# Optimization experiments

Measured on AMD Instinct MI355X. Metric: run time of the kernel, lower is better.

Reference implementation:

```python
import jax, jax.numpy as jnp
import numpy as np

LN_EPS = 1e-5


def _layer_norm(h, g, b):
    mu = jnp.mean(h, axis=-1, keepdims=True)
    var = jnp.mean((h - mu) ** 2, axis=-1, keepdims=True)
    return (h - mu) / jnp.sqrt(var + LN_EPS) * g + b


def setup_inputs() -> dict:
    key = jax.random.key(0)
    ks = jax.random.split(key, 12)
    B, N, D = 2, 2048, 768
    H, Dh = 12, 64
    Dp = D // 4  # 192, DynamicPositionBias width
    s = lambda fan_in: 1.0 / np.sqrt(fan_in)
    return {
        "x": jax.random.normal(ks[0], (B, N, D), jnp.float32),
        "qkv_w": jax.random.normal(ks[1], (D, 3 * H * Dh), jnp.float32) * s(D),
        "qkv_b": jax.random.normal(ks[2], (3 * H * Dh,), jnp.float32) * 0.02,
        "out_w": jax.random.normal(ks[3], (H * Dh, D), jnp.float32) * s(H * Dh),
        "out_b": jax.random.normal(ks[4], (D,), jnp.float32) * 0.02,
        "dpb_w_in": jax.random.normal(ks[5], (1, Dp), jnp.float32),
        "dpb_b_in": jax.random.normal(ks[6], (Dp,), jnp.float32) * 0.02,
        "dpb_w_hid": jax.random.normal(ks[7], (3, Dp, Dp), jnp.float32) * s(Dp),
        "dpb_b_hid": jax.random.normal(ks[8], (3, Dp), jnp.float32) * 0.02,
        "dpb_ln_g": jnp.ones((4, Dp), jnp.float32),
        "dpb_ln_b": jnp.zeros((4, Dp), jnp.float32),
        "dpb_w_out": jax.random.normal(ks[9], (Dp, 12), jnp.float32) * s(Dp),
        "dpb_b_out": jax.random.normal(ks[10], (12,), jnp.float32) * 0.02,
    }


def _dpb_bias(n, w_in, b_in, w_hid, b_hid, ln_g, ln_b, w_out, b_out):
    # positions -n+1 .. n-1, log-distance transform
    pos = jnp.arange(-n + 1, n, dtype=jnp.float32)[:, None]  # [2n-1, 1]
    pos = jnp.sign(pos) * jnp.log(jnp.abs(pos) + 1.0)
    h = jax.nn.silu(_layer_norm(pos @ w_in + b_in, ln_g[0], ln_b[0]))
    for l in range(3):
        h = jax.nn.silu(_layer_norm(h @ w_hid[l] + b_hid[l], ln_g[l + 1], ln_b[l + 1]))
    vals = h @ w_out + b_out  # [2n-1, H]
    idx = jnp.arange(n)[:, None] - jnp.arange(n)[None, :] + (n - 1)  # [n, n]
    bias = vals[idx]  # [n, n, H]
    return jnp.transpose(bias, (2, 0, 1))  # [H, n, n]


def reference(x, qkv_w, qkv_b, out_w, out_b,
              dpb_w_in, dpb_b_in, dpb_w_hid, dpb_b_hid,
              dpb_ln_g, dpb_ln_b, dpb_w_out, dpb_b_out):
    B, N, D = x.shape
    H = dpb_w_out.shape[-1]
    qkv = x @ qkv_w + qkv_b  # [B, N, 3*H*Dh]
    q, k, v = jnp.split(qkv, 3, axis=-1)
    split_heads = lambda t: jnp.transpose(t.reshape(B, N, H, -1), (0, 2, 1, 3))
    q, k, v = split_heads(q), split_heads(k), split_heads(v)  # [B, H, N, Dh]
    Dh = q.shape[-1]

    bias = _dpb_bias(N, dpb_w_in, dpb_b_in, dpb_w_hid, dpb_b_hid,
                     dpb_ln_g, dpb_ln_b, dpb_w_out, dpb_b_out)  # [H, N, N]

    scale = Dh ** -0.5
    sim = jnp.einsum("bhid,bhjd->bhij", q, k) * scale + bias[None]
    attn = jax.nn.softmax(sim, axis=-1)
    o = jnp.einsum("bhij,bhjd->bhid", attn, v)  # [B, H, N, Dh]
    o = jnp.transpose(o, (0, 2, 1, 3)).reshape(B, N, H * Dh)
    return o @ out_w + out_b
```

## Files before the change

### kernel.cpp

```cpp
#include <hip/hip_runtime.h>
#include <stdint.h>
#include <stddef.h>

typedef __bf16 bf16;
typedef __bf16 bf16x8 __attribute__((ext_vector_type(8)));
typedef float floatx4 __attribute__((ext_vector_type(4)));

typedef __attribute__((address_space(1))) void as1_void;
typedef __attribute__((address_space(3))) void as3_void;

__device__ __forceinline__ void async_ld16(const void* g, void* l) {
    __builtin_amdgcn_global_load_lds((as1_void*)g, (as3_void*)l, 16, 0, 0);
}

__device__ __forceinline__ floatx4 mfma16(bf16x8 a, bf16x8 b, floatx4 c) {
    return __builtin_amdgcn_mfma_f32_16x16x32_bf16(a, b, c, 0, 0, 0);
}

__device__ __forceinline__ unsigned cvtpk_bf16(float lo, float hi) {
    unsigned r;
    asm("v_cvt_pk_bf16_f32 %0, %1, %2" : "=v"(r) : "v"(lo), "v"(hi));
    return r;
}
__device__ __forceinline__ void pl32swap(unsigned &a, unsigned &b) {
    asm("v_permlane32_swap_b32 %0, %1" : "+v"(a), "+v"(b));
}
__device__ __forceinline__ void pl16swap(unsigned &a, unsigned &b) {
    asm("v_permlane16_swap_b32 %0, %1" : "+v"(a), "+v"(b));
}

#define LOG2E 1.4426950408889634f
#define SM_M2 24.0f
#define DP 192

__device__ __forceinline__ float ldsc(const void* p, size_t i, int isbf) {
    return isbf ? (float)((const bf16*)p)[i] : ((const float*)p)[i];
}
__device__ __forceinline__ bf16x8 ld8(const void* p, size_t i, int isbf) {
    if (isbf) return *(const bf16x8*)((const bf16*)p + i);
    const float* f = (const float*)p + i;
    float4 lo = *(const float4*)(f);
    float4 hi = *(const float4*)(f + 4);
    bf16x8 r;
    r[0]=(bf16)lo.x; r[1]=(bf16)lo.y; r[2]=(bf16)lo.z; r[3]=(bf16)lo.w;
    r[4]=(bf16)hi.x; r[5]=(bf16)hi.y; r[6]=(bf16)hi.z; r[7]=(bf16)hi.w;
    return r;
}
__device__ __forceinline__ int get_fl(const uint32_t* lng) {
    return (lng[0] == 0x3F803F80u) ? 1 : 0;
}

__device__ void transpose_body(const void* in, bf16* out, int R, int C,
                               int bx, int by, int fl, bf16 (*tile)[65]) {
    int c0 = bx * 64, r0 = by * 64;
    for (int i = threadIdx.x; i < 512; i += 256) {
        int rr = i >> 3, cc8 = (i & 7) * 8;
        int gr = r0 + rr, gc = c0 + cc8;
        if (gr < R && gc + 7 < C) {
            bf16x8 v = ld8(in, (size_t)gr * C + gc, fl);
            #pragma unroll
            for (int e = 0; e < 8; e++) tile[rr][cc8 + e] = v[e];
        } else {
            #pragma unroll
            for (int e = 0; e < 8; e++) {
                int gce = gc + e;
                tile[rr][cc8 + e] = (gr < R && gce < C)
                    ? (bf16)ldsc(in, (size_t)gr * C + gce, fl) : (bf16)0.0f;
            }
        }
    }
    __syncthreads();
    for (int i = threadIdx.x; i < 512; i += 256) {
        int cc = i >> 3, rr8 = (i & 7) * 8;
        int oR = c0 + cc, oC = r0 + rr8;
        if (oR < C && oC + 7 < R) {
            bf16x8 v;
            #pragma unroll
            for (int e = 0; e < 8; e++) v[e] = tile[rr8 + e][cc];
            *(bf16x8*)(out + (size_t)oR * R + oC) = v;
        } else if (oR < C) {
            #pragma unroll
            for (int e = 0; e < 8; e++)
                if (oC + e < R) out[(size_t)oR * R + oC + e] = tile[rr8 + e][cc];
        }
    }
}

__global__ __launch_bounds__(256) void prep_kernel(
    const void* __restrict__ qkv_w, const void* __restrict__ out_w,
    bf16* __restrict__ wt_qkv, bf16* __restrict__ wt_out,
    const void* __restrict__ w_hid, const void* __restrict__ w_out,
    bf16* __restrict__ WtH, bf16* __restrict__ Wt12,
    const uint32_t* __restrict__ lngw,
    const void* __restrict__ x, bf16* __restrict__ xbf)
{
    __shared__ bf16 tile[64][65];
    const int fl = get_fl(lngw);
    const int bid = blockIdx.x;
    if (bid < 432) {
        transpose_body(qkv_w, wt_qkv, 768, 2304, bid % 36, bid / 36, fl, tile);
        return;
    }
    if (bid < 576) {
        int b2 = bid - 432;
        transpose_body(out_w, wt_out, 768, 768, b2 % 12, b2 / 12, fl, tile);
        return;
    }
    if (bid < 603) {
        int b2 = bid - 576, l = b2 / 9, t9 = b2 % 9;
        transpose_body((const char*)w_hid + (size_t)l * DP * DP * (fl ? 2 : 4),
                       WtH + (size_t)l * DP * DP, DP, DP, t9 % 3, t9 / 3,
                       fl, tile);
        return;
    }
    if (bid < 606) {
        transpose_body(w_out, Wt12, 192, 12, 0, bid - 603, fl, tile);
        return;
    }
    size_t base = (size_t)(bid - 606) * 6144 + threadIdx.x * 8;
    #pragma unroll
    for (int c = 0; c < 3; c++)
        *(bf16x8*)(xbf + base + c*2048) = ld8(x, base + c*2048, fl);
}

#define GK 768
#define HS 200

__global__ __launch_bounds__(256) void gemm0_dpb_kernel(
    const bf16* __restrict__ A, const bf16* __restrict__ Bt,
    const void* __restrict__ bias, const uint32_t* __restrict__ lngw,
    bf16* __restrict__ out0, bf16* __restrict__ out1, bf16* __restrict__ out2,
    const void* __restrict__ w_in, const void* __restrict__ b_in,
    const void* __restrict__ b_hid, const void* __restrict__ ln_g,
    const void* __restrict__ ln_b, const void* __restrict__ b_out,
    const bf16* __restrict__ WtH, const bf16* __restrict__ Wt12,
    float* __restrict__ vals_t)
{
    __shared__ __align__(16) char smem[32768];
    const int fl = get_fl(lngw);
    const int tid = threadIdx.x;
    const int wave = tid >> 6, lane = tid & 63;
    const int g = lane >> 4, cl = lane & 15;

    if (blockIdx.x >= 576) {
        bf16*  Hb   = (bf16*)smem;
        float* redS = (float*)(smem + 6400);
        float* redQ = (float*)(smem + 6656);
        const int pbase = (blockIdx.x - 576) * 16;

        float tpos[4];
        #pragma unroll
        for (int rg = 0; rg < 4; rg++) {
            int p = pbase + g*4 + rg;
            float pv = (float)p - 2047.0f;
            float sg = (pv > 0.0f) ? 1.0f : ((pv < 0.0f) ? -1.0f : 0.0f);
            tpos[rg] = sg * logf(fabsf(pv) + 1.0f);
        }
        int col[3];
        #pragma unroll
        for (int tt = 0; tt < 3; tt++) col[tt] = (wave*3 + tt)*16 + cl;

        floatx4 acc[3];
        #pragma unroll
        for (int tt = 0; tt < 3; tt++) {
            float wi = ldsc(w_in, col[tt], fl), bi = ldsc(b_in, col[tt], fl);
            #pragma unroll
            for (int rg = 0; rg < 4; rg++) acc[tt][rg] = tpos[rg]*wi + bi;
        }

        #pragma unroll 1
        for (int l = 0; l < 4; l++) {
            float s1[4], s2[4];
            #pragma unroll
            for (int rg = 0; rg < 4; rg++) {
                s1[rg] = acc[0][rg] + acc[1][rg] + acc[2][rg];
                s2[rg] = acc[0][rg]*acc[0][rg] + acc[1][rg]*acc[1][rg]
                       + acc[2][rg]*acc[2][rg];
            }
            #pragma unroll
            for (int m = 1; m <= 8; m <<= 1)
                #pragma unroll
                for (int rg = 0; rg < 4; rg++) {
                    s1[rg] += __shfl_xor(s1[rg], m);
                    s2[rg] += __shfl_xor(s2[rg], m);
                }
            if (cl == 0)
                #pragma unroll
                for (int rg = 0; rg < 4; rg++) {
                    redS[wave*16 + g*4 + rg] = s1[rg];
                    redQ[wave*16 + g*4 + rg] = s2[rg];
                }
            __syncthreads();
            float mu[4], rstd[4];
            #pragma unroll
            for (int rg = 0; rg < 4; rg++) {
                int row = g*4 + rg;
                float S = redS[row] + redS[16+row] + redS[32+row] + redS[48+row];
                float Q = redQ[row] + redQ[16+row] + redQ[32+row] + redQ[48+row];
                float m_ = S * (1.0f/DP);
                float v_ = Q * (1.0f/DP) - m_*m_;
                mu[rg] = m_;
                rstd[rg] = 1.0f / sqrtf(v_ + 1e-5f);
            }
            #pragma unroll
            for (int tt = 0; tt < 3; tt++) {
                float ga = ldsc(ln_g, l*DP + col[tt], fl);
                float be = ldsc(ln_b, l*DP + col[tt], fl);
                #pragma unroll
                for (int rg = 0; rg < 4; rg++) {
                    float y = (acc[tt][rg] - mu[rg]) * rstd[rg] * ga + be;
                    float sil = y / (1.0f + __expf(-y));
                    Hb[(g*4 + rg)*HS + col[tt]] = (bf16)sil;
                }
            }
            __syncthreads();
            if (l == 3) break;
            #pragma unroll
            for (int tt = 0; tt < 3; tt++) {
                float bh = ldsc(b_hid, l*DP + col[tt], fl);
                #pragma unroll
                for (int rg = 0; rg < 4; rg++) acc[tt][rg] = bh;
            }
            const bf16* Wl = WtH + (size_t)l * DP * DP;
            #pragma unroll
            for (int ks = 0; ks < 6; ks++) {
                bf16x8 af = *(const bf16x8*)(Hb + cl*HS + ks*32 + g*8);
                #pragma unroll
                for (int tt = 0; tt < 3; tt++) {
                    bf16x8 bfv = *(const bf16x8*)(Wl + (size_t)col[tt]*DP
                                                  + ks*32 + g*8);
                    acc[tt] = mfma16(af, bfv, acc[tt]);
                }
            }
        }
        if (wave == 0) {
            floatx4 facc = {};
            if (cl < 12) {
                float bo = ldsc(b_out, cl, fl);
                #pragma unroll
                for (int rg = 0; rg < 4; rg++) facc[rg] = bo;
            }
            #pragma unroll
            for (int ks = 0; ks < 6; ks++) {
                bf16x8 af = *(const bf16x8*)(Hb + cl*HS + ks*32 + g*8);
                bf16x8 bfv = {};
                if (cl < 12)
                    bfv = *(const bf16x8*)(Wt12 + (size_t)cl*DP + ks*32 + g*8);
                facc = mfma16(af, bfv, facc);
            }
            if (cl < 12)
                #pragma unroll
                for (int rg = 0; rg < 4; rg++) {
                    int p = pbase + g*4 + rg;
                    if (p < 4095) vals_t[cl*4095 + p] = facc[rg];
                }
        }
        return;
    }

    bf16* Sb = (bf16*)smem;
    const int xcd8 = blockIdx.x & 7, slot = blockIdx.x >> 3;
    const int m0 = (xcd8*4 + slot/18) * 128, n0 = (slot % 18) * 128;
    const int wm = (wave >> 1) * 64, wn = (wave & 1) * 64;

    const int e0 = wave*512 + lane*8;
    const int e1 = e0 + 2048;
    const int r0 = e0 >> 5, c0e = e0 & 31;
    const int r1 = e1 >> 5, c1e = e1 & 31;
    const bf16* Ag0 = A  + (size_t)(m0 + r0) * GK + c0e;
    const bf16* Ag1 = A  + (size_t)(m0 + r1) * GK + c1e;
    const bf16* Bg0 = Bt + (size_t)(n0 + r0) * GK + c0e;
    const bf16* Bg1 = Bt + (size_t)(n0 + r1) * GK + c1e;

    const int frow = lane & 15, fk = (lane >> 4) * 8;
    floatx4 acc[4][4] = {};

    auto stage = [&](int t, int p) {
        const int k0 = t * 32;
        bf16* d = Sb + p * 8192;
        async_ld16(Ag0 + k0, d + e0);
        async_ld16(Ag1 + k0, d + e1);
        async_ld16(Bg0 + k0, d + 4096 + e0);
        async_ld16(Bg1 + k0, d + 4096 + e1);
    };

    stage(0, 0);
    __syncthreads();
    for (int t = 0; t < GK/32; ++t) {
        const int cur = t & 1;
        if (t + 1 < GK/32) stage(t + 1, cur ^ 1);
        const bf16* Ac = Sb + cur*8192;
        const bf16* Bc = Ac + 4096;
        bf16x8 af[4], bfr[4];
        #pragma unroll
        for (int i = 0; i < 4; i++)
            af[i] = *(const bf16x8*)(Ac + (wm + i*16 + frow)*32 + fk);
        #pragma unroll
        for (int j = 0; j < 4; j++)
            bfr[j] = *(const bf16x8*)(Bc + (wn + j*16 + frow)*32 + fk);
        #pragma unroll
        for (int i = 0; i < 4; i++)
            #pragma unroll
            for (int j = 0; j < 4; j++)
                acc[i][j] = mfma16(af[i], bfr[j], acc[i][j]);
        __syncthreads();
    }

    if (n0 >= 1536) {
        #pragma unroll
        for (int j = 0; j < 4; j++) {
            int Cc = n0 + wn + j*16 + cl;
            float bv = ldsc(bias, Cc, fl);
            int c2 = Cc - 1536, hh = c2 >> 6, dd = c2 & 63;
            #pragma unroll
            for (int kst = 0; kst < 2; kst++) {
                unsigned e0p = cvtpk_bf16(acc[2*kst][j][0] + bv,
                                          acc[2*kst][j][1] + bv);
                unsigned e1p = cvtpk_bf16(acc[2*kst][j][2] + bv,
                                          acc[2*kst][j][3] + bv);
                unsigned f0p = cvtpk_bf16(acc[2*kst+1][j][0] + bv,
                                          acc[2*kst+1][j][1] + bv);
                unsigned f1p = cvtpk_bf16(acc[2*kst+1][j][2] + bv,
                                          acc[2*kst+1][j][3] + bv);
                pl32swap(e0p, f0p); pl16swap(e0p, f0p);
                pl32swap(e1p, f1p); pl16swap(e1p, f1p);
                union { unsigned u[4]; bf16x8 v; } uu;
                uu.u[0] = e0p; uu.u[1] = e1p; uu.u[2] = f0p; uu.u[3] = f1p;
                int R0 = m0 + wm + kst*32 + g*8;
                int bb = R0 >> 11, nn = R0 & 2047;
                *(bf16x8*)(out2 + (((size_t)(bb*12 + hh) * 64 + dd) * 2048)
                           + nn) = uu.v;
            }
        }
        return;
    }

    #pragma unroll
    for (int i = 0; i < 4; i++) {
        #pragma unroll
        for (int j = 0; j < 4; j++) {
            int Cc = n0 + wn + j*16 + cl;
            float bv = ldsc(bias, Cc, fl);
            #pragma unroll
            for (int rg = 0; rg < 4; rg++) {
                int R = m0 + wm + i*16 + g*4 + rg;
                float val = acc[i][j][rg] + bv;
                int which = Cc / 768;
                int c2 = Cc - which * 768;
                int hh = c2 >> 6, dd = c2 & 63;
                int bb = R >> 11, nn = R & 2047;
                bf16* dst = (which == 0) ? out0 : out1;
                dst[((size_t)(bb*12 + hh) * 2048 + nn) * 64 + dd] = (bf16)val;
            }
        }
    }
}

__global__ __launch_bounds__(256) void gemm_out(
    const bf16* __restrict__ A, const bf16* __restrict__ Bt,
    const void* __restrict__ bias, const uint32_t* __restrict__ lngw,
    void* __restrict__ out0)
{
    __shared__ __align__(16) bf16 Sb[2][4096];
    const int fl  = get_fl(lngw);
    const int tid = threadIdx.x;
    const int wave = tid >> 6, lane = tid & 63;
    const int m0 = blockIdx.y * 64, n0 = blockIdx.x * 64;
    const int wm = (wave >> 1) * 32, wn = (wave & 1) * 32;

    const int e0 = tid * 8;
    const int r0 = e0 >> 5, c0e = e0 & 31;
    const bf16* Ag0 = A  + (size_t)(m0 + r0) * GK + c0e;
    const bf16* Bg0 = Bt + (size_t)(n0 + r0) * GK + c0e;

    const int frow = lane & 15, fk = (lane >> 4) * 8;
    floatx4 acc[2][2] = {};

    auto stage = [&](int t, int p) {
        const int k0 = t * 32;
        async_ld16(Ag0 + k0, &Sb[p][e0]);
        async_ld16(Bg0 + k0, &Sb[p][2048 + e0]);
    };

    stage(0, 0);
    __syncthreads();
    for (int t = 0; t < GK/32; ++t) {
        const int cur = t & 1;
        if (t + 1 < GK/32) stage(t + 1, cur ^ 1);
        const bf16* Ac = Sb[cur];
        const bf16* Bc = Ac + 2048;
        bf16x8 af[2], bfr[2];
        #pragma unroll
        for (int i = 0; i < 2; i++)
            af[i] = *(const bf16x8*)(Ac + (wm + i*16 + frow)*32 + fk);
        #pragma unroll
        for (int j = 0; j < 2; j++)
            bfr[j] = *(const bf16x8*)(Bc + (wn + j*16 + frow)*32 + fk);
        #pragma unroll
        for (int i = 0; i < 2; i++)
            #pragma unroll
            for (int j = 0; j < 2; j++)
                acc[i][j] = mfma16(af[i], bfr[j], acc[i][j]);
        __syncthreads();
    }

    const int g = lane >> 4, cl = lane & 15;
    #pragma unroll
    for (int i = 0; i < 2; i++) {
        #pragma unroll
        for (int j = 0; j < 2; j++) {
            int Cc = n0 + wn + j*16 + cl;
            float bv = ldsc(bias, Cc, fl);
            #pragma unroll
            for (int rg = 0; rg < 4; rg++) {
                int R = m0 + wm + i*16 + g*4 + rg;
                float val = acc[i][j][rg] + bv;
                size_t oi = (size_t)R * 768 + Cc;
                if (fl) ((bf16*)out0)[oi]  = (bf16)val;
                else    ((float*)out0)[oi] = val;
            }
        }
    }
}

__global__ __launch_bounds__(256) void attn_kernel(
    const bf16* __restrict__ qws, const bf16* __restrict__ kws,
    const bf16* __restrict__ vwst, const float* __restrict__ vals_t,
    bf16* __restrict__ ows)
{
    __shared__ __align__(16) bf16 Qs[64*72];
    __shared__ __align__(16) bf16 Ks[2][64*72];
    __shared__ __align__(16) bf16 Vt[2][64*72];
    __shared__ float bias_s[2][128];

    const int tid = threadIdx.x;
    const int wave = tid >> 6, lane = tid & 63;
    const int g = lane >> 4, cl = lane & 15;
    const int xcd8 = blockIdx.x & 7, slot = blockIdx.x >> 3;
    const int bh_ = xcd8*3 + (slot >> 5);
    const int q0 = (slot & 31) * 64;
    const int h = bh_ % 12, b = bh_ / 12;
    const size_t bh = (size_t)bh_;
    const bf16* qp  = qws  + bh * 2048 * 64;
    const bf16* kp  = kws  + bh * 2048 * 64;
    const bf16* vpt = vwst + bh * 64 * 2048;
    const float* vrow = vals_t + h * 4095;

    for (int i = tid; i < 512; i += 256) {
        int r = i >> 3, c = (i & 7) * 8;
        *(bf16x8*)(Qs + r*72 + c) = *(const bf16x8*)(qp + (size_t)(q0 + r)*64 + c);
    }

    const int sr0 = tid >> 3, sc0 = (tid & 7) * 8;
    const int sr1 = sr0 + 32;

    bf16x8 kreg0 = *(const bf16x8*)(kp + (size_t)sr0 * 64 + sc0);
    bf16x8 kreg1 = *(const bf16x8*)(kp + (size_t)sr1 * 64 + sc0);
    bf16x8 vreg0 = *(const bf16x8*)(vpt + (size_t)sr0 * 2048 + sc0);
    bf16x8 vreg1 = *(const bf16x8*)(vpt + (size_t)sr1 * 2048 + sc0);
    float  breg  = 0.0f;
    if (tid < 127) breg = vrow[q0 + 1984 + tid];
    *(bf16x8*)(Ks[0] + sr0*72 + sc0) = kreg0;
    *(bf16x8*)(Ks[0] + sr1*72 + sc0) = kreg1;
    *(bf16x8*)(Vt[0] + sr0*72 + sc0) = vreg0;
    *(bf16x8*)(Vt[0] + sr1*72 + sc0) = vreg1;
    if (tid < 127) bias_s[0][tid] = breg * LOG2E - SM_M2;

    kreg0 = *(const bf16x8*)(kp + (size_t)(64 + sr0) * 64 + sc0);
    kreg1 = *(const bf16x8*)(kp + (size_t)(64 + sr1) * 64 + sc0);
    vreg0 = *(const bf16x8*)(vpt + (size_t)sr0 * 2048 + 64 + sc0);
    vreg1 = *(const bf16x8*)(vpt + (size_t)sr1 * 2048 + 64 + sc0);
    if (tid < 127) breg = vrow[q0 - 64 + 1984 + tid];

    __syncthreads();
    bf16x8 aq0 = *(const bf16x8*)(Qs + (wave*16 + cl)*72 + g*8);
    bf16x8 aq1 = *(const bf16x8*)(Qs + (wave*16 + cl)*72 + 32 + g*8);

    floatx4 accO[4] = {};
    float lsum = 0.0f;
    const int il_b = wave*16 + g*4;
    const float c1 = 0.125f * LOG2E;
    const int bbase = wave*16 + cl - 4*g + 63;

    for (int j = 0; j < 32; ++j) {
        const int cur = j & 1;
        if (j + 1 < 32) {
            bf16* Kn = Ks[cur ^ 1];
            bf16* Vn = Vt[cur ^ 1];
            *(bf16x8*)(Kn + sr0*72 + sc0) = kreg0;
            *(bf16x8*)(Kn + sr1*72 + sc0) = kreg1;
            *(bf16x8*)(Vn + sr0*72 + sc0) = vreg0;
            *(bf16x8*)(Vn + sr1*72 + sc0) = vreg1;
            if (tid < 127) bias_s[cur ^ 1][tid] = breg * LOG2E - SM_M2;
        }
        if (j + 2 < 32) {
            const int nj = (j + 2) * 64;
            kreg0 = *(const bf16x8*)(kp + (size_t)(nj + sr0) * 64 + sc0);
            kreg1 = *(const bf16x8*)(kp + (size_t)(nj + sr1) * 64 + sc0);
            vreg0 = *(const bf16x8*)(vpt + (size_t)sr0 * 2048 + nj + sc0);
            vreg1 = *(const bf16x8*)(vpt + (size_t)sr1 * 2048 + nj + sc0);
            if (tid < 127) breg = vrow[q0 - nj + 1984 + tid];
        }

        const bf16* Kc = Ks[cur];
        const bf16* Vc = Vt[cur];
        const float* bs = bias_s[cur];

        floatx4 accS[4];
        #pragma unroll
        for (int jt = 0; jt < 4; jt++) {
            bf16x8 ak0 = *(const bf16x8*)(Kc + (jt*16 + cl)*72 + g*8);
            bf16x8 ak1 = *(const bf16x8*)(Kc + (jt*16 + cl)*72 + 32 + g*8);
            floatx4 z = {};
            z = mfma16(ak0, aq0, z);
            z = mfma16(ak1, aq1, z);
            accS[jt] = z;
        }

        unsigned pk[4][2];
        #pragma unroll
        for (int jt = 0; jt < 4; jt++) {
            float pv[4];
            #pragma unroll
            for (int rg = 0; rg < 4; rg++) {
                float x2 = fmaf(accS[jt][rg], c1, bs[bbase - jt*16 - rg]);
                x2 = fminf(x2, 80.0f);
                pv[rg] = __builtin_amdgcn_exp2f(x2);
            }
            lsum += (pv[0] + pv[1]) + (pv[2] + pv[3]);
            pk[jt][0] = cvtpk_bf16(pv[0], pv[1]);
            pk[jt][1] = cvtpk_bf16(pv[2], pv[3]);
        }

        bf16x8 ap[2];
        #pragma unroll
        for (int kst = 0; kst < 2; kst++) {
            unsigned e0p = pk[2*kst][0], f0p = pk[2*kst+1][0];
            unsigned e1p = pk[2*kst][1], f1p = pk[2*kst+1][1];
            pl32swap(e0p, f0p);
            pl16swap(e0p, f0p);
            pl32swap(e1p, f1p);
            pl16swap(e1p, f1p);
            union { unsigned u[4]; bf16x8 v; } uu;
            uu.u[0] = e0p; uu.u[1] = e1p; uu.u[2] = f0p; uu.u[3] = f1p;
            ap[kst] = uu.v;
        }

        #pragma unroll
        for (int dt = 0; dt < 4; dt++) {
            #pragma unroll
            for (int kst = 0; kst < 2; kst++) {
                bf16x8 bv = *(const bf16x8*)(Vc + (dt*16 + cl)*72 + kst*32 + g*8);
                accO[dt] = mfma16(ap[kst], bv, accO[dt]);
            }
        }

        __syncthreads();
    }

    lsum += __shfl_xor(lsum, 16);
    lsum += __shfl_xor(lsum, 32);

    #pragma unroll
    for (int rg = 0; rg < 4; rg++) {
        float l = __shfl(lsum, g*4 + rg);
        float inv = 1.0f / l;
        size_t row = (size_t)(b*2048 + q0 + il_b + rg) * 768 + h*64;
        #pragma unroll
        for (int dt = 0; dt < 4; dt++)
            ows[row + dt*16 + cl] = (bf16)(accO[dt][rg] * inv);
    }
}

extern "C" void kernel_launch(void* const* d_in, const int* in_sizes, int n_in,
                              void* d_out, int out_size, void* d_ws, size_t ws_size,
                              hipStream_t stream)
{
    (void)in_sizes; (void)n_in; (void)out_size;
    const void* x     = d_in[0];
    const void* qkv_w = d_in[1];
    const void* qkv_b = d_in[2];
    const void* out_w = d_in[3];
    const void* out_b = d_in[4];
    const void* w_in  = d_in[5];
    const void* b_in  = d_in[6];
    const void* w_hid = d_in[7];
    const void* b_hid = d_in[8];
    const void* ln_g  = d_in[9];
    const void* ln_b  = d_in[10];
    const void* w_out = d_in[11];
    const void* b_out = d_in[12];

    const size_t NEED = 4915200 + 4ull*6291456;
    if (ws_size < NEED) return;

    char* ws = (char*)d_ws;
    float* vals_t = (float*)(ws);
    bf16*  wt_qkv = (bf16*)(ws + 196608);
    bf16*  wt_out = (bf16*)(ws + 196608 + 3538944);
    bf16*  q_ws   = (bf16*)(ws + 4915200);
    bf16*  k_ws   = (bf16*)(ws + 4915200 + 6291456);
    bf16*  v_wst  = (bf16*)(ws + 4915200 + 2*6291456);
    bf16*  o_ws   = (bf16*)(ws + 4915200 + 3*6291456);
    bf16*  x_bf   = o_ws;
    bf16*  WtH    = (bf16*)d_out;
    bf16*  Wt12   = WtH + 3*DP*DP;

    prep_kernel<<<1118, 256, 0, stream>>>(qkv_w, out_w, wt_qkv, wt_out,
                                          w_hid, w_out, WtH, Wt12,
                                          (const uint32_t*)ln_g, x, x_bf);
    gemm0_dpb_kernel<<<832, 256, 0, stream>>>(
        x_bf, wt_qkv, qkv_b, (const uint32_t*)ln_g, q_ws, k_ws, v_wst,
        w_in, b_in, b_hid, ln_g, ln_b, b_out, WtH, Wt12, vals_t);
    attn_kernel<<<768, 256, 0, stream>>>(q_ws, k_ws, v_wst, vals_t, o_ws);
    gemm_out<<<dim3(12, 64), 256, 0, stream>>>(o_ws, wt_out, out_b,
                                               (const uint32_t*)ln_g, d_out);
}
```

Baseline: 194.4 us.

## Halve attention block to two waves, each computing 32 query rows

The attention kernel now runs 128 threads (2 waves) per block instead of 256, and each wave handles two 16-row query tiles. Each K/V fragment read from shared memory then feeds twice as many MFMAs, which cuts LDS read traffic per FLOP. Each thread now stages four K and four V vectors per tile instead of two. The cost is higher register pressure and fewer waves per block for hiding latency, which may lower occupancy or overlap.

```diff
diff --git a/kernel.cpp b/kernel.cpp
--- a/kernel.cpp
+++ b/kernel.cpp
@@ -423,7 +423,7 @@
     }
 }
 
-__global__ __launch_bounds__(256) void attn_kernel(
+__global__ __launch_bounds__(128) void attn_kernel(
     const bf16* __restrict__ qws, const bf16* __restrict__ kws,
     const bf16* __restrict__ vwst, const float* __restrict__ vals_t,
     bf16* __restrict__ ows)
@@ -446,59 +446,66 @@
     const bf16* vpt = vwst + bh * 64 * 2048;
     const float* vrow = vals_t + h * 4095;
 
-    for (int i = tid; i < 512; i += 256) {
+    for (int i = tid; i < 512; i += 128) {
         int r = i >> 3, c = (i & 7) * 8;
         *(bf16x8*)(Qs + r*72 + c) = *(const bf16x8*)(qp + (size_t)(q0 + r)*64 + c);
     }
 
     const int sr0 = tid >> 3, sc0 = (tid & 7) * 8;
-    const int sr1 = sr0 + 32;
-
-    bf16x8 kreg0 = *(const bf16x8*)(kp + (size_t)sr0 * 64 + sc0);
-    bf16x8 kreg1 = *(const bf16x8*)(kp + (size_t)sr1 * 64 + sc0);
-    bf16x8 vreg0 = *(const bf16x8*)(vpt + (size_t)sr0 * 2048 + sc0);
-    bf16x8 vreg1 = *(const bf16x8*)(vpt + (size_t)sr1 * 2048 + sc0);
-    float  breg  = 0.0f;
+
+    bf16x8 kr[4], vr[4];
+    #pragma unroll
+    for (int c = 0; c < 4; c++) {
+        kr[c] = *(const bf16x8*)(kp + (size_t)(sr0 + c*16) * 64 + sc0);
+        vr[c] = *(const bf16x8*)(vpt + (size_t)(sr0 + c*16) * 2048 + sc0);
+    }
+    float breg = 0.0f;
     if (tid < 127) breg = vrow[q0 + 1984 + tid];
-    *(bf16x8*)(Ks[0] + sr0*72 + sc0) = kreg0;
-    *(bf16x8*)(Ks[0] + sr1*72 + sc0) = kreg1;
-    *(bf16x8*)(Vt[0] + sr0*72 + sc0) = vreg0;
-    *(bf16x8*)(Vt[0] + sr1*72 + sc0) = vreg1;
+    #pragma unroll
+    for (int c = 0; c < 4; c++) {
+        *(bf16x8*)(Ks[0] + (sr0 + c*16)*72 + sc0) = kr[c];
+        *(bf16x8*)(Vt[0] + (sr0 + c*16)*72 + sc0) = vr[c];
+    }
     if (tid < 127) bias_s[0][tid] = breg * LOG2E - SM_M2;
 
-    kreg0 = *(const bf16x8*)(kp + (size_t)(64 + sr0) * 64 + sc0);
-    kreg1 = *(const bf16x8*)(kp + (size_t)(64 + sr1) * 64 + sc0);
-    vreg0 = *(const bf16x8*)(vpt + (size_t)sr0 * 2048 + 64 + sc0);
-    vreg1 = *(const bf16x8*)(vpt + (size_t)sr1 * 2048 + 64 + sc0);
+    #pragma unroll
+    for (int c = 0; c < 4; c++) {
+        kr[c] = *(const bf16x8*)(kp + (size_t)(64 + sr0 + c*16) * 64 + sc0);
+        vr[c] = *(const bf16x8*)(vpt + (size_t)(sr0 + c*16) * 2048 + 64 + sc0);
+    }
     if (tid < 127) breg = vrow[q0 - 64 + 1984 + tid];
 
     __syncthreads();
-    bf16x8 aq0 = *(const bf16x8*)(Qs + (wave*16 + cl)*72 + g*8);
-    bf16x8 aq1 = *(const bf16x8*)(Qs + (wave*16 + cl)*72 + 32 + g*8);
-
-    floatx4 accO[4] = {};
-    float lsum = 0.0f;
-    const int il_b = wave*16 + g*4;
+    bf16x8 aq0 = *(const bf16x8*)(Qs + (wave*32 + cl)*72 + g*8);
+    bf16x8 aq1 = *(const bf16x8*)(Qs + (wave*32 + cl)*72 + 32 + g*8);
+    bf16x8 aq2 = *(const bf16x8*)(Qs + (wave*32 + 16 + cl)*72 + g*8);
+    bf16x8 aq3 = *(const bf16x8*)(Qs + (wave*32 + 16 + cl)*72 + 32 + g*8);
+
+    floatx4 accO0[4] = {}, accO1[4] = {};
+    float lsum0 = 0.0f, lsum1 = 0.0f;
     const float c1 = 0.125f * LOG2E;
-    const int bbase = wave*16 + cl - 4*g + 63;
+    const int bbase0 = wave*32 + cl - 4*g + 63;
+    const int bbase1 = bbase0 + 16;
 
     for (int j = 0; j < 32; ++j) {
         const int cur = j & 1;
         if (j + 1 < 32) {
             bf16* Kn = Ks[cur ^ 1];
             bf16* Vn = Vt[cur ^ 1];
-            *(bf16x8*)(Kn + sr0*72 + sc0) = kreg0;
-            *(bf16x8*)(Kn + sr1*72 + sc0) = kreg1;
-            *(bf16x8*)(Vn + sr0*72 + sc0) = vreg0;
-            *(bf16x8*)(Vn + sr1*72 + sc0) = vreg1;
+            #pragma unroll
+            for (int c = 0; c < 4; c++) {
+                *(bf16x8*)(Kn + (sr0 + c*16)*72 + sc0) = kr[c];
+                *(bf16x8*)(Vn + (sr0 + c*16)*72 + sc0) = vr[c];
+            }
             if (tid < 127) bias_s[cur ^ 1][tid] = breg * LOG2E - SM_M2;
         }
         if (j + 2 < 32) {
             const int nj = (j + 2) * 64;
-            kreg0 = *(const bf16x8*)(kp + (size_t)(nj + sr0) * 64 + sc0);
-            kreg1 = *(const bf16x8*)(kp + (size_t)(nj + sr1) * 64 + sc0);
-            vreg0 = *(const bf16x8*)(vpt + (size_t)sr0 * 2048 + nj + sc0);
-            vreg1 = *(const bf16x8*)(vpt + (size_t)sr1 * 2048 + nj + sc0);
+            #pragma unroll
+            for (int c = 0; c < 4; c++) {
+                kr[c] = *(const bf16x8*)(kp + (size_t)(nj + sr0 + c*16) * 64 + sc0);
+                vr[c] = *(const bf16x8*)(vpt + (size_t)(sr0 + c*16) * 2048 + nj + sc0);
+            }
             if (tid < 127) breg = vrow[q0 - nj + 1984 + tid];
         }
 
@@ -506,44 +513,62 @@
         const bf16* Vc = Vt[cur];
         const float* bs = bias_s[cur];
 
-        floatx4 accS[4];
+        floatx4 accS0[4], accS1[4];
         #pragma unroll
         for (int jt = 0; jt < 4; jt++) {
             bf16x8 ak0 = *(const bf16x8*)(Kc + (jt*16 + cl)*72 + g*8);
             bf16x8 ak1 = *(const bf16x8*)(Kc + (jt*16 + cl)*72 + 32 + g*8);
-            floatx4 z = {};
-            z = mfma16(ak0, aq0, z);
-            z = mfma16(ak1, aq1, z);
-            accS[jt] = z;
-        }
-
-        unsigned pk[4][2];
+            floatx4 z0 = {}, z1 = {};
+            z0 = mfma16(ak0, aq0, z0);
+            z0 = mfma16(ak1, aq1, z0);
+            z1 = mfma16(ak0, aq2, z1);
+            z1 = mfma16(ak1, aq3, z1);
+            accS0[jt] = z0;
+            accS1[jt] = z1;
+        }
+
+        unsigned pk0[4][2], pk1[4][2];
         #pragma unroll
         for (int jt = 0; jt < 4; jt++) {
-            float pv[4];
+            float pv0[4], pv1[4];
             #pragma unroll
             for (int rg = 0; rg < 4; rg++) {
-                float x2 = fmaf(accS[jt][rg], c1, bs[bbase - jt*16 - rg]);
-                x2 = fminf(x2, 80.0f);
-                pv[rg] = __builtin_amdgcn_exp2f(x2);
-            }
-            lsum += (pv[0] + pv[1]) + (pv[2] + pv[3]);
-            pk[jt][0] = cvtpk_bf16(pv[0], pv[1]);
-            pk[jt][1] = cvtpk_bf16(pv[2], pv[3]);
-        }
-
-        bf16x8 ap[2];
+                float x0 = fmaf(accS0[jt][rg], c1, bs[bbase0 - jt*16 - rg]);
+                float x1 = fmaf(accS1[jt][rg], c1, bs[bbase1 - jt*16 - rg]);
+                x0 = fminf(x0, 80.0f);
+                x1 = fminf(x1, 80.0f);
+                pv0[rg] = __builtin_amdgcn_exp2f(x0);
+                pv1[rg] = __builtin_amdgcn_exp2f(x1);
+            }
+            lsum0 += (pv0[0] + pv0[1]) + (pv0[2] + pv0[3]);
+            lsum1 += (pv1[0] + pv1[1]) + (pv1[2] + pv1[3]);
+            pk0[jt][0] = cvtpk_bf16(pv0[0], pv0[1]);
+            pk0[jt][1] = cvtpk_bf16(pv0[2], pv0[3]);
+            pk1[jt][0] = cvtpk_bf16(pv1[0], pv1[1]);
+            pk1[jt][1] = cvtpk_bf16(pv1[2], pv1[3]);
+        }
+
+        bf16x8 ap0[2], ap1[2];
         #pragma unroll
         for (int kst = 0; kst < 2; kst++) {
-            unsigned e0p = pk[2*kst][0], f0p = pk[2*kst+1][0];
-            unsigned e1p = pk[2*kst][1], f1p = pk[2*kst+1][1];
-            pl32swap(e0p, f0p);
-            pl16swap(e0p, f0p);
-            pl32swap(e1p, f1p);
-            pl16swap(e1p, f1p);
-            union { unsigned u[4]; bf16x8 v; } uu;
-            uu.u[0] = e0p; uu.u[1] = e1p; uu.u[2] = f0p; uu.u[3] = f1p;
-            ap[kst] = uu.v;
+            {
+                unsigned e0p = pk0[2*kst][0], f0p = pk0[2*kst+1][0];
+                unsigned e1p = pk0[2*kst][1], f1p = pk0[2*kst+1][1];
+                pl32swap(e0p, f0p); pl16swap(e0p, f0p);
+                pl32swap(e1p, f1p); pl16swap(e1p, f1p);
+                union { unsigned u[4]; bf16x8 v; } uu;
+                uu.u[0] = e0p; uu.u[1] = e1p; uu.u[2] = f0p; uu.u[3] = f1p;
+                ap0[kst] = uu.v;
+            }
+            {
+                unsigned e0p = pk1[2*kst][0], f0p = pk1[2*kst+1][0];
+                unsigned e1p = pk1[2*kst][1], f1p = pk1[2*kst+1][1];
+                pl32swap(e0p, f0p); pl16swap(e0p, f0p);
+                pl32swap(e1p, f1p); pl16swap(e1p, f1p);
+                union { unsigned u[4]; bf16x8 v; } uu;
+                uu.u[0] = e0p; uu.u[1] = e1p; uu.u[2] = f0p; uu.u[3] = f1p;
+                ap1[kst] = uu.v;
+            }
         }
 
         #pragma unroll
@@ -551,24 +576,32 @@
             #pragma unroll
             for (int kst = 0; kst < 2; kst++) {
                 bf16x8 bv = *(const bf16x8*)(Vc + (dt*16 + cl)*72 + kst*32 + g*8);
-                accO[dt] = mfma16(ap[kst], bv, accO[dt]);
+                accO0[dt] = mfma16(ap0[kst], bv, accO0[dt]);
+                accO1[dt] = mfma16(ap1[kst], bv, accO1[dt]);
             }
         }
 
         __syncthreads();
     }
 
-    lsum += __shfl_xor(lsum, 16);
-    lsum += __shfl_xor(lsum, 32);
+    lsum0 += __shfl_xor(lsum0, 16);
+    lsum0 += __shfl_xor(lsum0, 32);
+    lsum1 += __shfl_xor(lsum1, 16);
+    lsum1 += __shfl_xor(lsum1, 32);
 
     #pragma unroll
     for (int rg = 0; rg < 4; rg++) {
-        float l = __shfl(lsum, g*4 + rg);
-        float inv = 1.0f / l;
-        size_t row = (size_t)(b*2048 + q0 + il_b + rg) * 768 + h*64;
-        #pragma unroll
-        for (int dt = 0; dt < 4; dt++)
-            ows[row + dt*16 + cl] = (bf16)(accO[dt][rg] * inv);
+        float l0 = __shfl(lsum0, g*4 + rg);
+        float l1 = __shfl(lsum1, g*4 + rg);
+        float inv0 = 1.0f / l0;
+        float inv1 = 1.0f / l1;
+        size_t row0 = (size_t)(b*2048 + q0 + wave*32 + g*4 + rg) * 768 + h*64;
+        size_t row1 = row0 + (size_t)16 * 768;
+        #pragma unroll
+        for (int dt = 0; dt < 4; dt++) {
+            ows[row0 + dt*16 + cl] = (bf16)(accO0[dt][rg] * inv0);
+            ows[row1 + dt*16 + cl] = (bf16)(accO1[dt][rg] * inv1);
+        }
     }
 }
 
@@ -612,7 +645,7 @@
     gemm0_dpb_kernel<<<832, 256, 0, stream>>>(
         x_bf, wt_qkv, qkv_b, (const uint32_t*)ln_g, q_ws, k_ws, v_wst,
         w_in, b_in, b_hid, ln_g, ln_b, b_out, WtH, Wt12, vals_t);
-    attn_kernel<<<768, 256, 0, stream>>>(q_ws, k_ws, v_wst, vals_t, o_ws);
+    attn_kernel<<<768, 128, 0, stream>>>(q_ws, k_ws, v_wst, vals_t, o_ws);
     gemm_out<<<dim3(12, 64), 256, 0, stream>>>(o_ws, wt_out, out_b,
                                                (const uint32_t*)ln_g, d_out);
 }
```

Measured after the change: 203.7 us. 1.05x slower.
